# Optimization experiments

Measured on AMD Instinct MI355X. Metric: run time of the kernel, lower is better.

The kernel has to match this reference:

```python
import jax, jax.numpy as jnp
import numpy as np

IN_DIM = 256
AT_DIM = 256
NUM_HEAD = 4
COMPRESS_QK = 8
D_QK = (AT_DIM // NUM_HEAD) // COMPRESS_QK  # 8, per-head qkv channels
AT_HEAD = AT_DIM // NUM_HEAD               # 64, per-head output channels
B, H, W = 2, 64, 64


def setup_inputs() -> dict:
    key = jax.random.key(0)
    ks = jax.random.split(key, 11)
    s = 0.02
    x = jax.random.normal(ks[0], (B, IN_DIM, H, W), dtype=jnp.float32)
    Wq = jax.random.normal(ks[1], (NUM_HEAD, D_QK, IN_DIM), dtype=jnp.float32) * s
    bq = jax.random.normal(ks[2], (NUM_HEAD, D_QK), dtype=jnp.float32) * s
    Wk = jax.random.normal(ks[3], (NUM_HEAD, D_QK, IN_DIM), dtype=jnp.float32) * s
    bk = jax.random.normal(ks[4], (NUM_HEAD, D_QK), dtype=jnp.float32) * s
    Wv = jax.random.normal(ks[5], (NUM_HEAD, D_QK, IN_DIM), dtype=jnp.float32) * s
    bv = jax.random.normal(ks[6], (NUM_HEAD, D_QK), dtype=jnp.float32) * s
    Wo = jax.random.normal(ks[7], (NUM_HEAD, AT_HEAD, D_QK), dtype=jnp.float32) * s
    bo = jax.random.normal(ks[8], (NUM_HEAD, AT_HEAD), dtype=jnp.float32) * s
    gamma = jax.random.normal(ks[9], (NUM_HEAD,), dtype=jnp.float32)  # torch inits 0; random for nontrivial test
    return {"x": x, "Wq": Wq, "bq": bq, "Wk": Wk, "bk": bk, "Wv": Wv,
            "bv": bv, "Wo": Wo, "bo": bo, "gamma": gamma}


def reference(x, Wq, bq, Wk, bk, Wv, bv, Wo, bo, gamma):
    b, C, h, w = x.shape
    N = h * w
    xf = x.reshape(b, C, N)  # flatten spatial -> [b, C, N]
    # 1x1 convs as channel contractions, all heads batched: [b, nh, d, N]
    q = jnp.einsum('hdc,bcn->bhdn', Wq, xf) + bq[None, :, :, None]
    k = jnp.einsum('hdc,bcn->bhdn', Wk, xf) + bk[None, :, :, None]
    v = jnp.einsum('hdc,bcn->bhdn', Wv, xf) + bv[None, :, :, None]
    # S[n,m] = sum_d q[d,n] * k[d,m]  (proj_query^T @ proj_key)
    S = jnp.einsum('bhdn,bhdm->bhnm', q, k)
    # torch softmax(dim=-2): normalize over rows n for each column m
    A = jax.nn.softmax(S, axis=-2)
    # proj_value @ attention_map_T : [b,h,d,m]
    o = jnp.einsum('bhdn,bhnm->bhdm', v, A)
    # out_conv 1x1: d -> AT_HEAD, then gamma scale
    y = jnp.einsum('hed,bhdm->bhem', Wo, o) + bo[None, :, :, None]
    y = gamma[None, :, None, None] * y
    # concat heads along channel dim, add residual
    out = y.reshape(b, NUM_HEAD * AT_HEAD, h, w) + x
    return out
```

## Files before the change

kernel.cpp:

```cpp
#include <hip/hip_runtime.h>
#include <hip/hip_bf16.h>

#define IN_DIM 256
#define NH 4
#define DQK 8
#define ATH 64
#define NB 2
#define NSP 4096
#define LOG2E 1.44269504088896f
#define LN2 0.6931471805599453f

typedef __attribute__((ext_vector_type(8))) short short8;
typedef __attribute__((ext_vector_type(16))) float f32x16;

#define Q_OFF 0
#define K_OFF (512u * 1024u)
#define V_OFF (1024u * 1024u)
#define P_OFF (3u * 1024u * 1024u)

__device__ __forceinline__ float fast_exp2(float x) {
#if __has_builtin(__builtin_amdgcn_exp2f)
    return __builtin_amdgcn_exp2f(x);
#else
    return __expf(x * LN2);
#endif
}

__device__ __forceinline__ unsigned short f2bf(float f) {
    __hip_bfloat16 t = __float2bfloat16(f);
    return *(unsigned short*)&t;
}

__global__ __launch_bounds__(64, 4) void qkv_kernel(
    const float* __restrict__ x,
    const float* __restrict__ Wq, const float* __restrict__ bq,
    const float* __restrict__ Wk, const float* __restrict__ bk,
    const float* __restrict__ Wv, const float* __restrict__ bv,
    unsigned char* __restrict__ ws)
{
    const int n = blockIdx.x * 64 + threadIdx.x;
    const int g = blockIdx.y;
    const int b = blockIdx.z;
    const int h = g / 3, sel = g % 3;

    const float* W = (sel == 0) ? Wq : (sel == 1) ? Wk : Wv;
    const float* bias = (sel == 0) ? bq : (sel == 1) ? bk : bv;

    float acc[DQK];
#pragma unroll
    for (int d = 0; d < DQK; ++d) acc[d] = bias[h * DQK + d];

    const float* xb = x + (size_t)b * IN_DIM * NSP + n;
    const float* Wh = W + h * DQK * IN_DIM;

#pragma unroll 8
    for (int c = 0; c < IN_DIM; ++c) {
        const float xv = xb[(size_t)c * NSP];
#pragma unroll
        for (int d = 0; d < DQK; ++d)
            acc[d] = fmaf(Wh[d * IN_DIM + c], xv, acc[d]);
    }

    const int bh = b * NH + h;
    if (sel == 2) {
        const int T = n >> 5, c2 = (n >> 4) & 1, h2 = (n >> 3) & 1, j = n & 7;
        unsigned char* base = ws + V_OFF + (size_t)bh * 262144u +
                              ((size_t)((T * 2 + c2) * 64 + 32 * h2) * 16) + j * 2;
#pragma unroll
        for (int e = 0; e < 8; ++e)
            *(unsigned short*)(base + e * 16) = f2bf(acc[e]);
        *(unsigned short*)(base + 8 * 16) = 0x3F80;
    } else {
        const float scale = (sel == 1) ? LOG2E : 1.0f;
        unsigned short r[8];
#pragma unroll
        for (int d = 0; d < DQK; ++d) r[d] = f2bf(acc[d] * scale);
        uint4 pk;
        pk.x = (unsigned)r[0] | ((unsigned)r[1] << 16);
        pk.y = (unsigned)r[2] | ((unsigned)r[3] << 16);
        pk.z = (unsigned)r[4] | ((unsigned)r[5] << 16);
        pk.w = (unsigned)r[6] | ((unsigned)r[7] << 16);
        unsigned char* base = ws + ((sel == 0) ? Q_OFF : K_OFF) +
                              ((size_t)bh * NSP + n) * 16;
        *(uint4*)base = pk;
    }
}

__global__ __launch_bounds__(64, 4) void attn_partial(unsigned char* __restrict__ ws)
{
    const int lane = threadIdx.x;
    const int mt = blockIdx.x;
    const int bh = blockIdx.y;
    const int nq = blockIdx.z;
    const int e = lane & 31;
    const int hp = lane >> 5;

    union U4 { uint4 u; short8 s; };
    const uint4 zero4 = make_uint4(0, 0, 0, 0);

    U4 kf;
    kf.u = (hp == 0)
        ? *(const uint4*)(ws + K_OFF + ((size_t)bh * NSP + mt * 32 + e) * 16)
        : zero4;

    const uint4* qrows = (const uint4*)(ws + Q_OFF + (size_t)bh * NSP * 16);
    const uint4* vfr = (const uint4*)(ws + V_OFF + (size_t)bh * 262144u);

    f32x16 acc = {};
    const f32x16 zc = {};

    const int nt0 = nq * 32;
    U4 qf_n, vf0_n, vf1_n;
    qf_n.u = (hp == 0) ? qrows[nt0 * 32 + e] : zero4;
    vf0_n.u = vfr[(nt0 * 2 + 0) * 64 + lane];
    vf1_n.u = vfr[(nt0 * 2 + 1) * 64 + lane];

    for (int t = 0; t < 32; ++t) {
        U4 qf = qf_n, vf0 = vf0_n, vf1 = vf1_n;
        if (t < 31) {
            const int nt = nt0 + t + 1;
            qf_n.u = (hp == 0) ? qrows[nt * 32 + e] : zero4;
            vf0_n.u = vfr[(nt * 2 + 0) * 64 + lane];
            vf1_n.u = vfr[(nt * 2 + 1) * 64 + lane];
        }

        f32x16 S = __builtin_amdgcn_mfma_f32_32x32x16_bf16(qf.s, kf.s, zc, 0, 0, 0);

        unsigned int Qd[8];
#pragma unroll
        for (int i = 0; i < 8; ++i) {
            const float a = fast_exp2(S[2 * i]);
            const float b2 = fast_exp2(S[2 * i + 1]);
            Qd[i] = (unsigned)f2bf(a) | ((unsigned)f2bf(b2) << 16);
        }

        const int sA0 = hp ? Qd[0] : Qd[2];
        const int sA1 = hp ? Qd[1] : Qd[3];
        const int rA0 = __shfl_xor(sA0, 32, 64);
        const int rA1 = __shfl_xor(sA1, 32, 64);
        const int sB0 = hp ? Qd[4] : Qd[6];
        const int sB1 = hp ? Qd[5] : Qd[7];
        const int rB0 = __shfl_xor(sB0, 32, 64);
        const int rB1 = __shfl_xor(sB1, 32, 64);

        U4 f0, f1;
        f0.u = hp ? make_uint4(rA0, rA1, Qd[2], Qd[3])
                  : make_uint4(Qd[0], Qd[1], rA0, rA1);
        f1.u = hp ? make_uint4(rB0, rB1, Qd[6], Qd[7])
                  : make_uint4(Qd[4], Qd[5], rB0, rB1);

        acc = __builtin_amdgcn_mfma_f32_32x32x16_bf16(f0.s, vf0.s, acc, 0, 0, 0);
        acc = __builtin_amdgcn_mfma_f32_32x32x16_bf16(f1.s, vf1.s, acc, 0, 0, 0);
    }

    if (e <= 8) {
        float* pp = (float*)(ws + P_OFF) +
                    ((((size_t)bh * 128 + mt) * 4 + nq) * 18 + hp * 9 + e) * 16;
#pragma unroll
        for (int r = 0; r < 16; ++r) pp[r] = acc[r];
    }
}

__global__ __launch_bounds__(256) void attn_epilogue(
    const unsigned char* __restrict__ ws,
    const float* __restrict__ x,
    const float* __restrict__ Wo, const float* __restrict__ bo,
    const float* __restrict__ gamma,
    float* __restrict__ out)
{
    __shared__ float sO[128 * 13];
    const int tid = threadIdx.x;
    const int ms = blockIdx.x;
    const int bh = blockIdx.y;
    const int h = bh & (NH - 1);
    const int b = bh >> 2;

    const float* P = (const float*)(ws + P_OFF);
    for (int idx = tid; idx < 128 * 9; idx += 256) {
        const int m_l = idx / 9, e = idx % 9;
        const int mt = ms * 4 + (m_l >> 5);
        const int m32 = m_l & 31;
        const int hp = (m32 >> 2) & 1;
        const int r = (m32 & 3) + 4 * (m32 >> 3);
        const size_t base = ((((size_t)bh * 128 + mt) * 4) * 18 + hp * 9 + e) * 16 + r;
        const float s = P[base] + P[base + 18 * 16] +
                        P[base + 2 * 18 * 16] + P[base + 3 * 18 * 16];
        sO[m_l * 13 + e] = s;
    }
    __syncthreads();

    const int m_l = tid & 127;
    const int half = tid >> 7;
    const float rl = 1.0f / sO[m_l * 13 + 8];
    float od[DQK];
#pragma unroll
    for (int d = 0; d < DQK; ++d) od[d] = sO[m_l * 13 + d] * rl;

    const float g = gamma[h];
    const int mg = ms * 128 + m_l;
#pragma unroll
    for (int eo = half * 32; eo < half * 32 + 32; ++eo) {
        const float* wo = Wo + (h * ATH + eo) * DQK;
        float y = bo[h * ATH + eo];
#pragma unroll
        for (int d = 0; d < DQK; ++d) y = fmaf(wo[d], od[d], y);
        const size_t oi = ((size_t)(b * IN_DIM) + h * ATH + eo) * NSP + mg;
        out[oi] = fmaf(g, y, x[oi]);
    }
}

extern "C" void kernel_launch(void* const* d_in, const int* in_sizes, int n_in,
                              void* d_out, int out_size, void* d_ws, size_t ws_size,
                              hipStream_t stream)
{
    const float* x = (const float*)d_in[0];
    const float* Wq = (const float*)d_in[1];
    const float* bq = (const float*)d_in[2];
    const float* Wk = (const float*)d_in[3];
    const float* bk = (const float*)d_in[4];
    const float* Wv = (const float*)d_in[5];
    const float* bv = (const float*)d_in[6];
    const float* Wo = (const float*)d_in[7];
    const float* bo = (const float*)d_in[8];
    const float* gamma = (const float*)d_in[9];
    float* out = (float*)d_out;
    unsigned char* ws = (unsigned char*)d_ws;

    qkv_kernel<<<dim3(NSP / 64, 12, NB), 64, 0, stream>>>(
        x, Wq, bq, Wk, bk, Wv, bv, ws);
    attn_partial<<<dim3(128, NB * NH, 4), 64, 0, stream>>>(ws);
    attn_epilogue<<<dim3(32, NB * NH), 256, 0, stream>>>(
        ws, x, Wo, bo, gamma, out);
}
```

Measured before the change: 131.6 us.

## Compute QKV projection with bf16 MFMA and add separate V fragment layout pass

```diff
diff --git a/kernel.cpp b/kernel.cpp
--- a/kernel.cpp
+++ b/kernel.cpp
@@ -8,82 +8,150 @@
 #define NB 2
 #define NSP 4096
 #define LOG2E 1.44269504088896f
-#define LN2 0.6931471805599453f
 
 typedef __attribute__((ext_vector_type(8))) short short8;
 typedef __attribute__((ext_vector_type(16))) float f32x16;
 
-#define Q_OFF 0
+#define Q_OFF 0u
 #define K_OFF (512u * 1024u)
-#define V_OFF (1024u * 1024u)
-#define P_OFF (3u * 1024u * 1024u)
+#define VR_OFF (1024u * 1024u)
+#define VF_OFF (1536u * 1024u)
+#define P_OFF (3584u * 1024u)
 
 __device__ __forceinline__ float fast_exp2(float x) {
 #if __has_builtin(__builtin_amdgcn_exp2f)
     return __builtin_amdgcn_exp2f(x);
 #else
-    return __expf(x * LN2);
+    return exp2f(x);
 #endif
 }
 
-__device__ __forceinline__ unsigned short f2bf(float f) {
-    __hip_bfloat16 t = __float2bfloat16(f);
-    return *(unsigned short*)&t;
-}
-
-__global__ __launch_bounds__(64, 4) void qkv_kernel(
+__device__ __forceinline__ unsigned bf_rne(float f) {
+    unsigned u = __float_as_uint(f);
+    u += 0x7FFFu + ((u >> 16) & 1u);
+    return u >> 16;
+}
+__device__ __forceinline__ unsigned pack2bf(float a, float b) {
+    return bf_rne(a) | (bf_rne(b) << 16);
+}
+__device__ __forceinline__ unsigned pack2bf_tr(float a, float b) {
+    return (__float_as_uint(a) >> 16) | (__float_as_uint(b) & 0xFFFF0000u);
+}
+
+__global__ __launch_bounds__(64) void qkv_gemm(
     const float* __restrict__ x,
     const float* __restrict__ Wq, const float* __restrict__ bq,
     const float* __restrict__ Wk, const float* __restrict__ bk,
     const float* __restrict__ Wv, const float* __restrict__ bv,
     unsigned char* __restrict__ ws)
 {
-    const int n = blockIdx.x * 64 + threadIdx.x;
-    const int g = blockIdx.y;
-    const int b = blockIdx.z;
-    const int h = g / 3, sel = g % 3;
-
-    const float* W = (sel == 0) ? Wq : (sel == 1) ? Wk : Wv;
-    const float* bias = (sel == 0) ? bq : (sel == 1) ? bk : bv;
-
-    float acc[DQK];
-#pragma unroll
-    for (int d = 0; d < DQK; ++d) acc[d] = bias[h * DQK + d];
-
-    const float* xb = x + (size_t)b * IN_DIM * NSP + n;
-    const float* Wh = W + h * DQK * IN_DIM;
-
-#pragma unroll 8
-    for (int c = 0; c < IN_DIM; ++c) {
-        const float xv = xb[(size_t)c * NSP];
-#pragma unroll
-        for (int d = 0; d < DQK; ++d)
-            acc[d] = fmaf(Wh[d * IN_DIM + c], xv, acc[d]);
-    }
-
-    const int bh = b * NH + h;
-    if (sel == 2) {
-        const int T = n >> 5, c2 = (n >> 4) & 1, h2 = (n >> 3) & 1, j = n & 7;
-        unsigned char* base = ws + V_OFF + (size_t)bh * 262144u +
-                              ((size_t)((T * 2 + c2) * 64 + 32 * h2) * 16) + j * 2;
-#pragma unroll
-        for (int e = 0; e < 8; ++e)
-            *(unsigned short*)(base + e * 16) = f2bf(acc[e]);
-        *(unsigned short*)(base + 8 * 16) = 0x3F80;
-    } else {
-        const float scale = (sel == 1) ? LOG2E : 1.0f;
-        unsigned short r[8];
-#pragma unroll
-        for (int d = 0; d < DQK; ++d) r[d] = f2bf(acc[d] * scale);
-        uint4 pk;
-        pk.x = (unsigned)r[0] | ((unsigned)r[1] << 16);
-        pk.y = (unsigned)r[2] | ((unsigned)r[3] << 16);
-        pk.z = (unsigned)r[4] | ((unsigned)r[5] << 16);
-        pk.w = (unsigned)r[6] | ((unsigned)r[7] << 16);
-        unsigned char* base = ws + ((sel == 0) ? Q_OFF : K_OFF) +
-                              ((size_t)bh * NSP + n) * 16;
-        *(uint4*)base = pk;
-    }
+    const int lane = threadIdx.x;
+    const int nt = blockIdx.x;
+    const int mt = blockIdx.y;
+    const int b  = blockIdx.z;
+    const int col = lane & 31;
+    const int hp  = lane >> 5;
+
+    const int R = mt * 32 + col;
+    const int h = R / 24;
+    const int r24 = R % 24;
+    const int sel = r24 >> 3;
+    const int dd = r24 & 7;
+    const float* Wsel = (sel == 0) ? Wq : (sel == 1) ? Wk : Wv;
+    const float* wrow = Wsel + (h * DQK + dd) * IN_DIM;
+
+    const float* xb = x + (size_t)b * IN_DIM * NSP + (size_t)(hp * 8) * NSP + nt * 32 + col;
+
+    union U4 { uint4 u; short8 s; };
+    f32x16 acc = {};
+
+#pragma unroll
+    for (int kt = 0; kt < 16; ++kt) {
+        const float4 wa = *(const float4*)(wrow + kt * 16 + hp * 8);
+        const float4 wb = *(const float4*)(wrow + kt * 16 + hp * 8 + 4);
+        U4 af;
+        af.u.x = pack2bf(wa.x, wa.y);
+        af.u.y = pack2bf(wa.z, wa.w);
+        af.u.z = pack2bf(wb.x, wb.y);
+        af.u.w = pack2bf(wb.z, wb.w);
+
+        float xv[8];
+#pragma unroll
+        for (int j = 0; j < 8; ++j) xv[j] = xb[(size_t)(kt * 16 + j) * NSP];
+        U4 bfm;
+        bfm.u.x = pack2bf(xv[0], xv[1]);
+        bfm.u.y = pack2bf(xv[2], xv[3]);
+        bfm.u.z = pack2bf(xv[4], xv[5]);
+        bfm.u.w = pack2bf(xv[6], xv[7]);
+
+        acc = __builtin_amdgcn_mfma_f32_32x32x16_bf16(af.s, bfm.s, acc, 0, 0, 0);
+    }
+
+    const int n = nt * 32 + col;
+#pragma unroll
+    for (int p = 0; p < 2; ++p) {
+        const int gA = 2 * p, gB = 2 * p + 1;
+        const int RA = mt * 32 + 8 * gA, RB = mt * 32 + 8 * gB;
+        const int hA = RA / 24, hB = RB / 24;
+        const int selA = (RA % 24) >> 3, selB = (RB % 24) >> 3;
+        const float* bsA = (selA == 0) ? bq : (selA == 1) ? bk : bv;
+        const float* bsB = (selB == 0) ? bq : (selB == 1) ? bk : bv;
+        const float scA = (selA == 1) ? LOG2E : 1.0f;
+        const float scB = (selB == 1) ? LOG2E : 1.0f;
+
+        float vA[4], vB[4];
+#pragma unroll
+        for (int j = 0; j < 4; ++j) {
+            vA[j] = (acc[4 * gA + j] + bsA[hA * DQK + 4 * hp + j]) * scA;
+            vB[j] = (acc[4 * gB + j] + bsB[hB * DQK + 4 * hp + j]) * scB;
+        }
+        const unsigned PA0 = pack2bf(vA[0], vA[1]), PA1 = pack2bf(vA[2], vA[3]);
+        const unsigned PB0 = pack2bf(vB[0], vB[1]), PB1 = pack2bf(vB[2], vB[3]);
+
+        const int s0 = hp ? (int)PA0 : (int)PB0;
+        const int s1 = hp ? (int)PA1 : (int)PB1;
+        const unsigned r0 = (unsigned)__shfl_xor(s0, 32, 64);
+        const unsigned r1 = (unsigned)__shfl_xor(s1, 32, 64);
+
+        const uint4 row = hp ? make_uint4(r0, r1, PB0, PB1)
+                             : make_uint4(PA0, PA1, r0, r1);
+
+        const unsigned offA = (selA == 0) ? Q_OFF : (selA == 1) ? K_OFF : VR_OFF;
+        const unsigned offB = (selB == 0) ? Q_OFF : (selB == 1) ? K_OFF : VR_OFF;
+        unsigned char* dA = ws + offA + ((size_t)(b * NH + hA) * NSP + n) * 16;
+        unsigned char* dB = ws + offB + ((size_t)(b * NH + hB) * NSP + n) * 16;
+        *(uint4*)(hp ? dB : dA) = row;
+    }
+}
+
+__global__ __launch_bounds__(64) void vfrag_kernel(unsigned char* __restrict__ ws)
+{
+    const int tid = threadIdx.x;
+    if (tid >= 36) return;
+    const int T = blockIdx.x;
+    const int bh = blockIdx.y;
+    const int e = tid % 9;
+    const int r = tid / 9;
+    const int h2 = r & 1, c2 = r >> 1;
+
+    unsigned char* dst = ws + VF_OFF + (size_t)bh * 262144u +
+                         (size_t)((T * 2 + c2) * 64 + 32 * h2 + e) * 16;
+    if (e == 8) {
+        *(uint4*)dst = make_uint4(0x3F803F80u, 0x3F803F80u, 0x3F803F80u, 0x3F803F80u);
+        return;
+    }
+    const unsigned char* src = ws + VR_OFF +
+        ((size_t)bh * NSP + T * 32 + c2 * 16 + h2 * 8) * 16 + e * 2;
+    unsigned w0 = 0, w1 = 0, w2 = 0, w3 = 0;
+    w0 = (unsigned)*(const unsigned short*)(src + 0 * 16) |
+         ((unsigned)*(const unsigned short*)(src + 1 * 16) << 16);
+    w1 = (unsigned)*(const unsigned short*)(src + 2 * 16) |
+         ((unsigned)*(const unsigned short*)(src + 3 * 16) << 16);
+    w2 = (unsigned)*(const unsigned short*)(src + 4 * 16) |
+         ((unsigned)*(const unsigned short*)(src + 5 * 16) << 16);
+    w3 = (unsigned)*(const unsigned short*)(src + 6 * 16) |
+         ((unsigned)*(const unsigned short*)(src + 7 * 16) << 16);
+    *(uint4*)dst = make_uint4(w0, w1, w2, w3);
 }
 
 __global__ __launch_bounds__(64, 4) void attn_partial(unsigned char* __restrict__ ws)
@@ -104,7 +172,7 @@
         : zero4;
 
     const uint4* qrows = (const uint4*)(ws + Q_OFF + (size_t)bh * NSP * 16);
-    const uint4* vfr = (const uint4*)(ws + V_OFF + (size_t)bh * 262144u);
+    const uint4* vfr = (const uint4*)(ws + VF_OFF + (size_t)bh * 262144u);
 
     f32x16 acc = {};
     const f32x16 zc = {};
@@ -126,12 +194,12 @@
 
         f32x16 S = __builtin_amdgcn_mfma_f32_32x32x16_bf16(qf.s, kf.s, zc, 0, 0, 0);
 
-        unsigned int Qd[8];
+        unsigned Qd[8];
 #pragma unroll
         for (int i = 0; i < 8; ++i) {
             const float a = fast_exp2(S[2 * i]);
             const float b2 = fast_exp2(S[2 * i + 1]);
-            Qd[i] = (unsigned)f2bf(a) | ((unsigned)f2bf(b2) << 16);
+            Qd[i] = pack2bf_tr(a, b2);
         }
 
         const int sA0 = hp ? Qd[0] : Qd[2];
@@ -226,8 +294,9 @@
     float* out = (float*)d_out;
     unsigned char* ws = (unsigned char*)d_ws;
 
-    qkv_kernel<<<dim3(NSP / 64, 12, NB), 64, 0, stream>>>(
+    qkv_gemm<<<dim3(128, 3, NB), 64, 0, stream>>>(
         x, Wq, bq, Wk, bk, Wv, bv, ws);
+    vfrag_kernel<<<dim3(128, NB * NH), 64, 0, stream>>>(ws);
     attn_partial<<<dim3(128, NB * NH, 4), 64, 0, stream>>>(ws);
     attn_epilogue<<<dim3(32, NB * NH), 256, 0, stream>>>(
         ws, x, Wo, bo, gamma, out);
```

After: 119.9 us. 8.8% less time.
